# Performance work log

Measured on AMD Instinct MI355X. Metric: run time of the kernel, lower is better.

The kernel has to match this reference:

```python
import jax, jax.numpy as jnp
import numpy as np

N_SAMPLES = 131072
N_EVENTS = 128
N_ATOMS = 32
ATOM_SIZE = 512
LATENT_DIM = 16
TOTAL_LAYERS = 7  # log2(n_events)


def setup_inputs() -> dict:
    key = jax.random.key(0)
    ks = jax.random.split(key, 9)
    r = lambda k, s: jax.random.normal(k, s, dtype=jnp.float32) * 0.1
    return {
        "base_latent": r(ks[0], (1, LATENT_DIM)),
        "to_off_w": r(ks[1], (TOTAL_LAYERS, 2, LATENT_DIM)),
        "split_w": r(ks[2], (TOTAL_LAYERS, 2 * LATENT_DIM, LATENT_DIM)),
        "split_b": r(ks[3], (TOTAL_LAYERS, 2 * LATENT_DIM)),
        "atoms": r(ks[4], (N_ATOMS, ATOM_SIZE)),
        "to_atoms_w": r(ks[5], (N_ATOMS, LATENT_DIM)),
        "to_atoms_b": r(ks[6], (N_ATOMS,)),
        "to_amp_w": r(ks[7], (1, LATENT_DIM)),
        "to_amp_b": r(ks[8], (1,)),
    }


def fft_shift(a, shift):
    # FFT-based fractional delay: pad to 3*n, phase-rotate spectrum, crop.
    n = a.shape[-1]
    shift_samples = shift * n * 0.5  # shift: (B, E, 1)
    a = jnp.pad(a, [(0, 0)] * (a.ndim - 1) + [(0, n * 2)])
    spec = jnp.fft.rfft(a, axis=-1, norm="ortho")
    n_coeffs = spec.shape[-1]
    coeffs = (jnp.arange(n_coeffs) * 2j * jnp.pi) / n_coeffs  # (n_coeffs,)
    spec = spec * jnp.exp(coeffs * shift_samples)  # broadcast (B,E,n_coeffs)
    samples = jnp.fft.irfft(spec, axis=-1, norm="ortho")
    return samples[..., :n]


def _forward(base_latent, to_off_w, split_w, split_b, atoms,
             to_atoms_w, to_atoms_b, to_amp_w, to_amp_b):
    x = base_latent[:, None, :]                     # (1, 1, L)
    base_times = jnp.zeros((1, 1, 1), dtype=x.dtype)
    for i in range(TOTAL_LAYERS):
        scale = 1.0 / (2 ** i)
        b, e, _ = x.shape
        to = jax.nn.sigmoid(jnp.einsum("bel,ol->beo", x, to_off_w[i]))  # (b,e,2)
        base_times = (base_times + to * scale).reshape(b, e * 2, 1)
        split = jnp.einsum("bel,ol->beo", x, split_w[i]) + split_b[i]   # (b,e,2L)
        x = split.reshape(b, e * 2, LATENT_DIM)
    # x: (1, 128, L), base_times: (1, 128, 1)
    mix = jnp.einsum("bel,al->bea", x, to_atoms_w) + to_atoms_b          # (1,E,A)
    ev = jnp.einsum("bea,at->bet", mix, atoms)                           # (1,E,512)
    n_arr = jnp.arange(ATOM_SIZE, dtype=ev.dtype)
    window = 0.54 - 0.46 * jnp.cos(2.0 * jnp.pi * n_arr / ATOM_SIZE)     # periodic hamming
    ev = ev * window
    ev = jnp.pad(ev, ((0, 0), (0, 0), (0, N_SAMPLES - ATOM_SIZE)))       # (1,E,n_samples)
    ev = ev / (jnp.linalg.norm(ev, axis=-1, keepdims=True) + 1e-8)       # unit_norm
    amps = jnp.einsum("bel,ol->beo", x, to_amp_w) + to_amp_b             # (1,E,1)
    ev = ev * amps
    scheduled = fft_shift(ev, base_times)                                # (1,E,n_samples)
    return jnp.sum(scheduled, axis=1, keepdims=True)                     # (1,1,n_samples)


def reference(base_latent, to_off_w, split_w, split_b, atoms,
              to_atoms_w, to_atoms_b, to_amp_w, to_amp_b):
    return _forward(base_latent, to_off_w, split_w, split_b, atoms,
                    to_atoms_w, to_atoms_b, to_amp_w, to_amp_b)
```

## Files before the change

kernel.cpp:

```cpp
#include <hip/hip_runtime.h>
#include <hip/hip_bf16.h>
#include <math.h>

constexpr int NSAMP  = 131072;
constexpr int NEV    = 128;
constexpr int ASIZE  = 512;
constexpr int LDIM   = 16;
constexpr int NLAYER = 7;
constexpr int NFFT   = 393216;
constexpr int MHALF  = 196608;
constexpr double TWO_PI = 6.283185307179586;


__device__ __forceinline__ float2 cmulf(float2 a, float2 b) {
    return make_float2(a.x*b.x - a.y*b.y, a.x*b.y + a.y*b.x);
}
__device__ __forceinline__ float2 CADD(float2 a, float2 b){ return make_float2(a.x+b.x, a.y+b.y); }
__device__ __forceinline__ float2 CSUB(float2 a, float2 b){ return make_float2(a.x-b.x, a.y-b.y); }

__device__ __forceinline__ void phase_sc(float th32, float* ps, float* pc) {
    const double th = (double)th32;
    const double n  = rint(th * 0.15915494309189535);
    double r = fma(-n, 6.283185307179586, th);
    r = fma(-n, 2.4492935982947064e-16, r);
    __sincosf((float)r, ps, pc);
}

#define RT2 0.70710678118654752f
#define DFT8F(A0,A1,A2,A3,A4,A5,A6,A7, X0,X1,X2,X3,X4,X5,X6,X7) { \
  float2 b0=CADD(A0,A4), b1=CADD(A1,A5), b2=CADD(A2,A6), b3=CADD(A3,A7); \
  float2 c0=CSUB(A0,A4); \
  float2 d1=CSUB(A1,A5), d2=CSUB(A2,A6), d3=CSUB(A3,A7); \
  float2 c1=make_float2((d1.x+d1.y)*RT2, (d1.y-d1.x)*RT2); \
  float2 c2=make_float2(d2.y, -d2.x); \
  float2 c3=make_float2((d3.y-d3.x)*RT2, -(d3.x+d3.y)*RT2); \
  float2 t0=CADD(b0,b2), t1=CSUB(b0,b2), t2=CADD(b1,b3), t3=CSUB(b1,b3); \
  X0=CADD(t0,t2); X4=CSUB(t0,t2); \
  X2=make_float2(t1.x+t3.y, t1.y-t3.x); X6=make_float2(t1.x-t3.y, t1.y+t3.x); \
  t0=CADD(c0,c2); t1=CSUB(c0,c2); t2=CADD(c1,c3); t3=CSUB(c1,c3); \
  X1=CADD(t0,t2); X5=CSUB(t0,t2); \
  X3=make_float2(t1.x+t3.y, t1.y-t3.x); X7=make_float2(t1.x-t3.y, t1.y+t3.x); \
}

__global__ __launch_bounds__(256) void init_all(
    const float* __restrict__ base, const float* __restrict__ to_off_w,
    const float* __restrict__ split_w, const float* __restrict__ split_b,
    float* __restrict__ xF, float* __restrict__ sF,
    float2* __restrict__ Twf, float2* __restrict__ Ttab)
{
    const int blk = blockIdx.x;
    const int tid = threadIdx.x;
    if (blk == 0) {
        __shared__ float xA[NEV*LDIM], xB[NEV*LDIM], bA[NEV], bB[NEV];
        if (tid < LDIM) xA[tid] = base[tid];
        if (tid == 0) bA[0] = 0.0f;
        __syncthreads();
        float* xi = xA; float* xo = xB; float* bi = bA; float* bo = bB;
        for (int i = 0; i < NLAYER; ++i) {
            const int ein = 1 << i;
            const float scale = 1.0f / (float)(1 << i);
            for (int idx = tid; idx < ein*32; idx += 256) {
                const int ep = idx >> 5, o2 = idx & 31;
                const float* wr = split_w + (i*32 + o2)*LDIM;
                const float* xr = xi + ep*LDIM;
                float s = __fmul_rn(xr[0], wr[0]);
                for (int l = 1; l < LDIM; ++l)
                    s = __fadd_rn(s, __fmul_rn(xr[l], wr[l]));
                s = __fadd_rn(s, split_b[i*32 + o2]);
                xo[(ep*2 + (o2>>4))*LDIM + (o2&15)] = s;
            }
            for (int idx = tid; idx < ein*2; idx += 256) {
                const int ep = idx >> 1, o = idx & 1;
                const float* wr = to_off_w + (i*2 + o)*LDIM;
                const float* xr = xi + ep*LDIM;
                float v = __fmul_rn(xr[0], wr[0]);
                for (int l = 1; l < LDIM; ++l)
                    v = __fadd_rn(v, __fmul_rn(xr[l], wr[l]));
                const float ef = (float)exp(-(double)v);
                const float sg = __fdiv_rn(1.0f, __fadd_rn(1.0f, ef));
                bo[ep*2 + o] = __fadd_rn(bi[ep], __fmul_rn(sg, scale));
            }
            __syncthreads();
            float* t;
            t = xi; xi = xo; xo = t;
            t = bi; bi = bo; bo = t;
        }
        for (int idx = tid; idx < NEV*LDIM; idx += 256) xF[idx] = xi[idx];
        for (int e = tid; e < NEV; e += 256)
            sF[e] = __fmul_rn(__fmul_rn(bi[e], 131072.0f), 0.5f);
        return;
    }
    if (blk == 1) {
        double s, c;
        sincos(TWO_PI*(double)tid/256.0,   &s, &c); Twf[tid]       = make_float2((float)c,(float)s);
        sincos(TWO_PI*(double)tid/512.0,   &s, &c); Twf[256 + tid] = make_float2((float)c,(float)s);
        sincos(TWO_PI*(double)tid/768.0,   &s, &c); Twf[512 + tid] = make_float2((float)c,(float)s);
        sincos(TWO_PI*(double)tid/65536.0, &s, &c); Twf[768 + tid] = make_float2((float)c,(float)s);
        return;
    }
    const int b = blk - 2;
    for (int j = tid; j < 512; j += 256) {
        double s, c;
        sincos(-TWO_PI*(double)(b*j)/(double)NFFT, &s, &c);
        Ttab[b*512 + (j & 63)*8 + (j >> 6)] = make_float2((float)c, (float)s);
    }
}

__global__ __launch_bounds__(256) void events_f32(
    const float* __restrict__ atoms, const float* __restrict__ to_atoms_w,
    const float* __restrict__ to_atoms_b, const float* __restrict__ to_amp_w,
    const float* __restrict__ to_amp_b, const float* __restrict__ xF,
    float* __restrict__ zf)
{
    const int e = blockIdx.x;
    const int tid = threadIdx.x;
    __shared__ float mixS[32];
    __shared__ float evS[ASIZE];
    __shared__ double red[256];
    __shared__ float scl[2];
    const float* x = xF + e*LDIM;
    if (tid < 32) {
        const float* wr = to_atoms_w + tid*LDIM;
        float m = __fmul_rn(x[0], wr[0]);
        for (int l = 1; l < LDIM; ++l) m = __fadd_rn(m, __fmul_rn(x[l], wr[l]));
        mixS[tid] = __fadd_rn(m, to_atoms_b[tid]);
    }
    __syncthreads();
    double ss = 0.0;
    for (int u = tid; u < ASIZE; u += 256) {
        float v = __fmul_rn(mixS[0], atoms[u]);
        for (int a = 1; a < 32; ++a)
            v = __fadd_rn(v, __fmul_rn(mixS[a], atoms[a*ASIZE + u]));
        const float ang = __fdiv_rn(__fmul_rn(6.283185307179586f, (float)u), 512.0f);
        const float cw = (float)cos((double)ang);
        const float w  = __fsub_rn(0.54f, __fmul_rn(0.46f, cw));
        v = __fmul_rn(v, w);
        evS[u] = v;
        ss += (double)v * (double)v;
    }
    red[tid] = ss; __syncthreads();
    for (int s = 128; s > 0; s >>= 1) { if (tid < s) red[tid] += red[tid+s]; __syncthreads(); }
    if (tid == 0) {
        const float nf = (float)sqrt(red[0]);
        scl[0] = __fadd_rn(nf, 1e-8f);
        float a = __fmul_rn(x[0], to_amp_w[0]);
        for (int l = 1; l < LDIM; ++l) a = __fadd_rn(a, __fmul_rn(x[l], to_amp_w[l]));
        scl[1] = __fadd_rn(a, to_amp_b[0]);
    }
    __syncthreads();
    const float den = scl[0], amp = scl[1];
    for (int u = tid; u < ASIZE; u += 256)
        zf[e*ASIZE + (u & 63)*8 + (u >> 6)] =
            __fmul_rn(__fdiv_rn(evS[u], den), amp);
}

__global__ __launch_bounds__(256, 3) void forward_v3(
    const float* __restrict__ zf, const float* __restrict__ sF,
    const float2* __restrict__ Ttab, float* __restrict__ Hqf)
{
    __shared__ float2 FB[4*576];
    const int b       = blockIdx.x >> 2;
    const int quarter = blockIdx.x & 3;
    const int tid  = threadIdx.x;
    const int wave = tid >> 6, lane = tid & 63;
    float2* F = FB + wave*576;
    const int e0 = quarter*32;

    const float4* Tg4 = (const float4*)(Ttab + b*512 + lane*8);
    const float4 tA = Tg4[0], tB = Tg4[1], tC = Tg4[2], tD = Tg4[3];
    const float2 T0 = make_float2(tA.x, tA.y), T1 = make_float2(tA.z, tA.w);
    const float2 T2 = make_float2(tB.x, tB.y), T3 = make_float2(tB.z, tB.w);
    const float2 T4 = make_float2(tC.x, tC.y), T5 = make_float2(tC.z, tC.w);
    const float2 T6 = make_float2(tD.x, tD.y), T7 = make_float2(tD.z, tD.w);

    float2 w0b, w1b;
    __sincosf(-6.283185307179586f/512.0f * (float)lane,        &w0b.y, &w0b.x);
    __sincosf(-6.283185307179586f/64.0f  * (float)(lane >> 3), &w1b.y, &w1b.x);

    float c2a[4], c2b[4];
    #pragma unroll
    for (int j = 0; j < 4; ++j) {
        const int a  = lane + 64*j;
        const int k1 = b + 768*a;
        const int k2 = (768 - b) + 768*(255 - a);
        c2a[j] = __fdiv_rn(__fmul_rn((float)(2*k1), 3.14159274101257324f), 196609.0f);
        c2b[j] = __fdiv_rn(__fmul_rn((float)(2*k2), 3.14159274101257324f), 196609.0f);
    }

    float a1R[4]={0,0,0,0}, a1I[4]={0,0,0,0};
    float a2R[4]={0,0,0,0}, a2I[4]={0,0,0,0};
    const int ph = lane + (lane >> 3);

    const float4* zp4 = (const float4*)(zf + (e0 + wave*8)*ASIZE + lane*8);
    float4 za = zp4[0], zb = zp4[1];

    for (int it = 0; it < 8; ++it) {
        const float sev = sF[e0 + wave*8 + it];
        {
            const float2 i0 = make_float2(za.x*T0.x, za.x*T0.y);
            const float2 i1 = make_float2(za.y*T1.x, za.y*T1.y);
            const float2 i2 = make_float2(za.z*T2.x, za.z*T2.y);
            const float2 i3 = make_float2(za.w*T3.x, za.w*T3.y);
            const float2 i4 = make_float2(zb.x*T4.x, zb.x*T4.y);
            const float2 i5 = make_float2(zb.y*T5.x, zb.y*T5.y);
            const float2 i6 = make_float2(zb.z*T6.x, zb.z*T6.y);
            const float2 i7 = make_float2(zb.w*T7.x, zb.w*T7.y);
            za = zp4[(it+1)*128];
            zb = zp4[(it+1)*128 + 1];
            float2 x0,x1,x2,x3,x4,x5,x6,x7;
            DFT8F(i0,i1,i2,i3,i4,i5,i6,i7, x0,x1,x2,x3,x4,x5,x6,x7);
            const int ob = 9*lane;
            float2 wm = w0b;
            F[ob]   = x0;
            F[ob+1] = cmulf(x1, wm); wm = cmulf(wm, w0b);
            F[ob+2] = cmulf(x2, wm); wm = cmulf(wm, w0b);
            F[ob+3] = cmulf(x3, wm); wm = cmulf(wm, w0b);
            F[ob+4] = cmulf(x4, wm); wm = cmulf(wm, w0b);
            F[ob+5] = cmulf(x5, wm); wm = cmulf(wm, w0b);
            F[ob+6] = cmulf(x6, wm); wm = cmulf(wm, w0b);
            F[ob+7] = cmulf(x7, wm);
        }
        {
            const float2 i0 = F[ph      ], i1 = F[ph +  72], i2 = F[ph + 144],
                         i3 = F[ph + 216], i4 = F[ph + 288], i5 = F[ph + 360],
                         i6 = F[ph + 432], i7 = F[ph + 504];
            float2 x0,x1,x2,x3,x4,x5,x6,x7;
            DFT8F(i0,i1,i2,i3,i4,i5,i6,i7, x0,x1,x2,x3,x4,x5,x6,x7);
            const int q = lane & 7, p = lane >> 3;
            const int ob = q + 72*p;
            float2 wm = w1b;
            F[ob]    = x0;
            F[ob+ 9] = cmulf(x1, wm); wm = cmulf(wm, w1b);
            F[ob+18] = cmulf(x2, wm); wm = cmulf(wm, w1b);
            F[ob+27] = cmulf(x3, wm); wm = cmulf(wm, w1b);
            F[ob+36] = cmulf(x4, wm); wm = cmulf(wm, w1b);
            F[ob+45] = cmulf(x5, wm); wm = cmulf(wm, w1b);
            F[ob+54] = cmulf(x6, wm); wm = cmulf(wm, w1b);
            F[ob+63] = cmulf(x7, wm);
        }
        float2 Y[8];
        {
            const float2 i0 = F[ph      ], i1 = F[ph +  72], i2 = F[ph + 144],
                         i3 = F[ph + 216], i4 = F[ph + 288], i5 = F[ph + 360],
                         i6 = F[ph + 432], i7 = F[ph + 504];
            DFT8F(i0,i1,i2,i3,i4,i5,i6,i7, Y[0],Y[1],Y[2],Y[3],Y[4],Y[5],Y[6],Y[7]);
        }
        #pragma unroll
        for (int j = 0; j < 4; ++j) {
            float ps, pc;
            const float2 S0 = Y[j];
            phase_sc(__fmul_rn(c2a[j], sev), &ps, &pc);
            a1R[j] = fmaf(S0.x, pc, fmaf(-S0.y, ps, a1R[j]));
            a1I[j] = fmaf(S0.x, ps, fmaf( S0.y, pc, a1I[j]));
            const float2 S1 = Y[j+4];
            phase_sc(__fmul_rn(c2b[j], sev), &ps, &pc);
            a2R[j] = fmaf(S1.x, pc, fmaf( S1.y, ps, a2R[j]));
            a2I[j] = fmaf(S1.x, ps, fmaf(-S1.y, pc, a2I[j]));
        }
    }

    float* redF = (float*)FB;
    #pragma unroll
    for (int round = 0; round < 2; ++round) {
        __syncthreads();
        const int j0 = 2*round;
        float* my = redF + (wave*64 + lane)*8;
        my[0]=a1R[j0];   my[1]=a1I[j0];   my[2]=a2R[j0];   my[3]=a2I[j0];
        my[4]=a1R[j0+1]; my[5]=a1I[j0+1]; my[6]=a2R[j0+1]; my[7]=a2I[j0+1];
        __syncthreads();
        const int s = tid >> 2, c = tid & 3;
        #pragma unroll
        for (int jr = 0; jr < 2; ++jr) {
            float v = 0.f;
            #pragma unroll
            for (int w = 0; w < 4; ++w) v += redF[(w*64 + s)*8 + jr*4 + c];
            const int as = s + 64*(j0 + jr);
            if (c < 2) {
                Hqf[2*(quarter*196609 + b*256 + as) + c] = v;
            } else if (b != 384) {
                if (b != 0)
                    Hqf[2*(quarter*196609 + (768-b)*256 + (255-as)) + (c-2)] = v;
                else if (as == 0)
                    Hqf[2*(quarter*196609 + 196608) + (c-2)] = v;
            }
        }
    }
}

__device__ __forceinline__ void ifft256f_stage(
    const float2* __restrict__ src, float2* __restrict__ dst, int t, int s4,
    const float2* __restrict__ Tw256f)
{
    const int lg = 2*s4, st = 1 << lg;
    const int q = t & (st-1), p = t >> lg;
    const float2 A0 = src[t], A1 = src[t+64], A2 = src[t+128], A3 = src[t+192];
    const float Pr = A0.x + A2.x, Pi_ = A0.y + A2.y;
    const float Qr = A0.x - A2.x, Qi  = A0.y - A2.y;
    const float Rr = A1.x + A3.x, Ri  = A1.y + A3.y;
    const float Sr = A1.x - A3.x, Si  = A1.y - A3.y;
    const int tw = p*st;
    const float2 w1 = Tw256f[tw];
    const float2 w2 = Tw256f[(2*tw) & 255];
    const float2 w3 = Tw256f[(3*tw) & 255];
    const int o = q + 4*st*p;
    dst[o] = make_float2(Pr + Rr, Pi_ + Ri);
    const float u1r = Qr - Si, u1i = Qi + Sr;
    dst[o + st]   = make_float2(u1r*w1.x - u1i*w1.y, u1r*w1.y + u1i*w1.x);
    const float u2r = Pr - Rr, u2i = Pi_ - Ri;
    dst[o + 2*st] = make_float2(u2r*w2.x - u2i*w2.y, u2r*w2.y + u2i*w2.x);
    const float u3r = Qr + Si, u3i = Qi - Sr;
    dst[o + 3*st] = make_float2(u3r*w3.x - u3i*w3.y, u3r*w3.y + u3i*w3.x);
}

__global__ __launch_bounds__(64) void inv_a(
    const float* __restrict__ Hqf, const float2* __restrict__ Twf,
    float2* __restrict__ Yg)
{
    __shared__ float2 buf[512];
    const int t = threadIdx.x;
    const int job = blockIdx.x;
    const int l = job >> 8, j1 = job & 255;
    const int k0 = 3*j1 + l;
    float2* A = buf; float2* B = buf + 256;
    const float2* Hq2 = (const float2*)Hqf;
    const float2* Tw256f = Twf;
    const float2* Tw512f = Twf + 256;
    const float2* Tw64kf = Twf + 768;

    double Ss, Sc; sincos(TWO_PI*(double)k0/(double)NFFT, &Ss, &Sc);
    const float Scf = (float)Sc, Ssf = (float)Ss;

    #pragma unroll
    for (int r = 0; r < 4; ++r) {
        const int j2 = t + 64*r;
        const int idxK = k0*256 + j2;
        int idxM;
        if (k0 > 0) idxM = (768 - k0)*256 + (255 - j2);
        else        idxM = (j2 == 0) ? 196608 : (256 - j2);
        float hkR=0.f, hkI=0.f, hmR=0.f, hmI=0.f;
        #pragma unroll
        for (int q = 0; q < 4; ++q) {
            const float2 vk = Hq2[q*196609 + idxK];
            const float2 vm = Hq2[q*196609 + idxM];
            hkR += vk.x; hkI += vk.y;
            hmR += vm.x; hmI += vm.y;
        }
        if (k0 == 0 && j2 == 0) { hkI = 0.f; hmI = 0.f; }
        const float Pr = hkR + hmR, Pi_ = hkI - hmI;
        const float Qr = hkR - hmR, Qi = hkI + hmI;
        const float2 t5 = Tw512f[j2];
        const float Wc = Scf*t5.x - Ssf*t5.y;
        const float Wsn = Scf*t5.y + Ssf*t5.x;
        const float WQr = Wc*Qr - Wsn*Qi;
        const float WQi = Wc*Qi + Wsn*Qr;
        A[j2] = make_float2(0.5f*(Pr - WQi), 0.5f*(Pi_ + WQr));
    }

    ifft256f_stage(A, B, t, 0, Tw256f);
    ifft256f_stage(B, A, t, 1, Tw256f);
    ifft256f_stage(A, B, t, 2, Tw256f);
    ifft256f_stage(B, A, t, 3, Tw256f);

    #pragma unroll
    for (int r = 0; r < 4; ++r) {
        const int m1 = t + 64*r;
        const float2 v = A[m1];
        const int vv = j1*m1;
        const float2 wa = Tw256f[vv >> 8];
        const float2 wb = Tw64kf[vv & 255];
        const float twc = wa.x*wb.x - wa.y*wb.y;
        const float tws = wa.x*wb.y + wa.y*wb.x;
        Yg[m1*768 + job] = make_float2(v.x*twc - v.y*tws, v.x*tws + v.y*twc);
    }
}

__global__ __launch_bounds__(192) void inv_b(
    const float2* __restrict__ Yg, const float2* __restrict__ Twf,
    float* __restrict__ out)
{
    __shared__ float2 buf[3*512];
    const int m1 = blockIdx.x;
    const int tid = threadIdx.x;
    const int l = tid >> 6, t = tid & 63;
    const float2* Tw256f = Twf;
    const float2* Tw768f = Twf + 512;
    {
        float2* A = buf + l*512;
        float2* B = A + 256;
        #pragma unroll
        for (int r = 0; r < 4; ++r) {
            const int j1 = t + 64*r;
            A[j1] = Yg[m1*768 + l*256 + j1];
        }
        ifft256f_stage(A, B, t, 0, Tw256f);
        ifft256f_stage(B, A, t, 1, Tw256f);
        ifft256f_stage(A, B, t, 2, Tw256f);
        ifft256f_stage(B, A, t, 3, Tw256f);
    }
    __syncthreads();

    double smd, cmd; sincos(TWO_PI*(double)m1/(double)MHALF, &smd, &cmd);
    const float cm = (float)cmd, sm = (float)smd;
    const float inv = 1.0f/(float)MHALF;
    for (int m2 = tid; m2 < 256; m2 += 192) {
        const float2 F0 = buf[m2];
        const float2 F1 = buf[512 + m2];
        const float2 F2 = buf[1024 + m2];
        const float2 t7 = Tw768f[m2];
        const float w1c = cm*t7.x - sm*t7.y, w1s = cm*t7.y + sm*t7.x;
        const float w2c = w1c*w1c - w1s*w1s, w2s = 2.0f*w1c*w1s;
        const float gr = F0.x + (w1c*F1.x - w1s*F1.y) + (w2c*F2.x - w2s*F2.y);
        const float gi = F0.y + (w1c*F1.y + w1s*F1.x) + (w2c*F2.y + w2s*F2.x);
        const int m = m1 + 256*m2;
        out[2*m]     = gr*inv;
        out[2*m + 1] = gi*inv;
    }
}

extern "C" void kernel_launch(void* const* d_in, const int* in_sizes, int n_in,
                              void* d_out, int out_size, void* d_ws, size_t ws_size,
                              hipStream_t stream) {
    const float* base       = (const float*)d_in[0];
    const float* to_off_w   = (const float*)d_in[1];
    const float* split_w    = (const float*)d_in[2];
    const float* split_b    = (const float*)d_in[3];
    const float* atoms      = (const float*)d_in[4];
    const float* to_atoms_w = (const float*)d_in[5];
    const float* to_atoms_b = (const float*)d_in[6];
    const float* to_amp_w   = (const float*)d_in[7];
    const float* to_amp_b   = (const float*)d_in[8];
    float* out = (float*)d_out;

    char* ws = (char*)d_ws;
    float2* Twf  = (float2*)(ws + 0);
    float*  sF   = (float*)(ws + 8192);
    float*  xF   = (float*)(ws + 8704);
    float*  zf   = (float*)(ws + 16896);
    float2* Ttab = (float2*)(ws + 279040);
    float2* Yg   = (float2*)(ws + 279040);
    float*  Hqf  = (float*)(ws + 1856000);

    init_all<<<387, 256, 0, stream>>>(base, to_off_w, split_w, split_b,
                                      xF, sF, Twf, Ttab);
    events_f32<<<NEV, 256, 0, stream>>>(atoms, to_atoms_w, to_atoms_b,
                                        to_amp_w, to_amp_b, xF, zf);
    forward_v3<<<385*4, 256, 0, stream>>>(zf, sF, Ttab, Hqf);
    inv_a<<<768, 64, 0, stream>>>(Hqf, Twf, Yg);
    inv_b<<<256, 192, 0, stream>>>(Yg, Twf, out);
}
```

Before: 136.8 us.

## Fuse latent tree walk into events kernel and precompute per-block twiddles

Merges the init and events kernels into one launch. Each event block now recomputes its own path down the binary split tree (7 small matvecs) instead of waiting on a single block that builds all 128 latents. The double-precision sincos calls in inv_a and inv_b are replaced by lookups into small Tk/Tm tables filled by the init block. This removes one kernel launch and a serial single-block dependency, at the cost of redundant per-event tree computation and more global table reads.

```diff
diff --git a/kernel.cpp b/kernel.cpp
--- a/kernel.cpp
+++ b/kernel.cpp
@@ -42,87 +42,87 @@
   X3=make_float2(t1.x+t3.y, t1.y-t3.x); X7=make_float2(t1.x-t3.y, t1.y+t3.x); \
 }
 
-__global__ __launch_bounds__(256) void init_all(
+__global__ __launch_bounds__(256) void init_events(
     const float* __restrict__ base, const float* __restrict__ to_off_w,
     const float* __restrict__ split_w, const float* __restrict__ split_b,
-    float* __restrict__ xF, float* __restrict__ sF,
-    float2* __restrict__ Twf, float2* __restrict__ Ttab)
+    const float* __restrict__ atoms, const float* __restrict__ to_atoms_w,
+    const float* __restrict__ to_atoms_b, const float* __restrict__ to_amp_w,
+    const float* __restrict__ to_amp_b,
+    float* __restrict__ sF, float2* __restrict__ Twf,
+    float2* __restrict__ Ttab,
+    float2* __restrict__ Tk, float2* __restrict__ Tm,
+    float* __restrict__ zf)
 {
     const int blk = blockIdx.x;
     const int tid = threadIdx.x;
-    if (blk == 0) {
-        __shared__ float xA[NEV*LDIM], xB[NEV*LDIM], bA[NEV], bB[NEV];
-        if (tid < LDIM) xA[tid] = base[tid];
-        if (tid == 0) bA[0] = 0.0f;
-        __syncthreads();
-        float* xi = xA; float* xo = xB; float* bi = bA; float* bo = bB;
-        for (int i = 0; i < NLAYER; ++i) {
-            const int ein = 1 << i;
-            const float scale = 1.0f / (float)(1 << i);
-            for (int idx = tid; idx < ein*32; idx += 256) {
-                const int ep = idx >> 5, o2 = idx & 31;
-                const float* wr = split_w + (i*32 + o2)*LDIM;
-                const float* xr = xi + ep*LDIM;
-                float s = __fmul_rn(xr[0], wr[0]);
-                for (int l = 1; l < LDIM; ++l)
-                    s = __fadd_rn(s, __fmul_rn(xr[l], wr[l]));
-                s = __fadd_rn(s, split_b[i*32 + o2]);
-                xo[(ep*2 + (o2>>4))*LDIM + (o2&15)] = s;
-            }
-            for (int idx = tid; idx < ein*2; idx += 256) {
-                const int ep = idx >> 1, o = idx & 1;
-                const float* wr = to_off_w + (i*2 + o)*LDIM;
-                const float* xr = xi + ep*LDIM;
-                float v = __fmul_rn(xr[0], wr[0]);
-                for (int l = 1; l < LDIM; ++l)
-                    v = __fadd_rn(v, __fmul_rn(xr[l], wr[l]));
-                const float ef = (float)exp(-(double)v);
-                const float sg = __fdiv_rn(1.0f, __fadd_rn(1.0f, ef));
-                bo[ep*2 + o] = __fadd_rn(bi[ep], __fmul_rn(sg, scale));
-            }
-            __syncthreads();
-            float* t;
-            t = xi; xi = xo; xo = t;
-            t = bi; bi = bo; bo = t;
-        }
-        for (int idx = tid; idx < NEV*LDIM; idx += 256) xF[idx] = xi[idx];
-        for (int e = tid; e < NEV; e += 256)
-            sF[e] = __fmul_rn(__fmul_rn(bi[e], 131072.0f), 0.5f);
+    if (blk < 385) {
+        const int b = blk;
+        for (int j = tid; j < 512; j += 256) {
+            double s, c;
+            sincos(-TWO_PI*(double)(b*j)/(double)NFFT, &s, &c);
+            Ttab[b*512 + (j & 63)*8 + (j >> 6)] = make_float2((float)c, (float)s);
+        }
         return;
     }
-    if (blk == 1) {
+    if (blk == 385) {
         double s, c;
         sincos(TWO_PI*(double)tid/256.0,   &s, &c); Twf[tid]       = make_float2((float)c,(float)s);
         sincos(TWO_PI*(double)tid/512.0,   &s, &c); Twf[256 + tid] = make_float2((float)c,(float)s);
         sincos(TWO_PI*(double)tid/768.0,   &s, &c); Twf[512 + tid] = make_float2((float)c,(float)s);
         sincos(TWO_PI*(double)tid/65536.0, &s, &c); Twf[768 + tid] = make_float2((float)c,(float)s);
+        for (int k0 = tid; k0 < 768; k0 += 256) {
+            sincos(TWO_PI*(double)k0/(double)NFFT, &s, &c);
+            Tk[k0] = make_float2((float)c, (float)s);
+        }
+        {
+            sincos(TWO_PI*(double)tid/(double)MHALF, &s, &c);
+            Tm[tid] = make_float2((float)c, (float)s);
+        }
         return;
     }
-    const int b = blk - 2;
-    for (int j = tid; j < 512; j += 256) {
-        double s, c;
-        sincos(-TWO_PI*(double)(b*j)/(double)NFFT, &s, &c);
-        Ttab[b*512 + (j & 63)*8 + (j >> 6)] = make_float2((float)c, (float)s);
-    }
-}
-
-__global__ __launch_bounds__(256) void events_f32(
-    const float* __restrict__ atoms, const float* __restrict__ to_atoms_w,
-    const float* __restrict__ to_atoms_b, const float* __restrict__ to_amp_w,
-    const float* __restrict__ to_amp_b, const float* __restrict__ xF,
-    float* __restrict__ zf)
-{
-    const int e = blockIdx.x;
-    const int tid = threadIdx.x;
+
+    const int e = blk - 386;
+    __shared__ float xcur[LDIM], xnxt[LDIM];
+    __shared__ float btS;
     __shared__ float mixS[32];
     __shared__ float evS[ASIZE];
     __shared__ double red[256];
     __shared__ float scl[2];
-    const float* x = xF + e*LDIM;
+
+    if (tid < LDIM) xcur[tid] = base[tid];
+    if (tid == 0) btS = 0.0f;
+    __syncthreads();
+    for (int i = 0; i < NLAYER; ++i) {
+        const int j = (e >> (6 - i)) & 1;
+        const float scale = 1.0f / (float)(1 << i);
+        if (tid < LDIM) {
+            const float* wr = split_w + (i*32 + j*16 + tid)*LDIM;
+            float s = __fmul_rn(xcur[0], wr[0]);
+            for (int l = 1; l < LDIM; ++l)
+                s = __fadd_rn(s, __fmul_rn(xcur[l], wr[l]));
+            s = __fadd_rn(s, split_b[i*32 + j*16 + tid]);
+            xnxt[tid] = s;
+        }
+        if (tid == 64) {
+            const float* wr = to_off_w + (i*2 + j)*LDIM;
+            float v = __fmul_rn(xcur[0], wr[0]);
+            for (int l = 1; l < LDIM; ++l)
+                v = __fadd_rn(v, __fmul_rn(xcur[l], wr[l]));
+            const float ef = (float)exp(-(double)v);
+            const float sg = __fdiv_rn(1.0f, __fadd_rn(1.0f, ef));
+            btS = __fadd_rn(btS, __fmul_rn(sg, scale));
+        }
+        __syncthreads();
+        if (tid < LDIM) xcur[tid] = xnxt[tid];
+        __syncthreads();
+    }
+    if (tid == 0)
+        sF[e] = __fmul_rn(__fmul_rn(btS, 131072.0f), 0.5f);
+
     if (tid < 32) {
         const float* wr = to_atoms_w + tid*LDIM;
-        float m = __fmul_rn(x[0], wr[0]);
-        for (int l = 1; l < LDIM; ++l) m = __fadd_rn(m, __fmul_rn(x[l], wr[l]));
+        float m = __fmul_rn(xcur[0], wr[0]);
+        for (int l = 1; l < LDIM; ++l) m = __fadd_rn(m, __fmul_rn(xcur[l], wr[l]));
         mixS[tid] = __fadd_rn(m, to_atoms_b[tid]);
     }
     __syncthreads();
@@ -143,8 +143,8 @@
     if (tid == 0) {
         const float nf = (float)sqrt(red[0]);
         scl[0] = __fadd_rn(nf, 1e-8f);
-        float a = __fmul_rn(x[0], to_amp_w[0]);
-        for (int l = 1; l < LDIM; ++l) a = __fadd_rn(a, __fmul_rn(x[l], to_amp_w[l]));
+        float a = __fmul_rn(xcur[0], to_amp_w[0]);
+        for (int l = 1; l < LDIM; ++l) a = __fadd_rn(a, __fmul_rn(xcur[l], to_amp_w[l]));
         scl[1] = __fadd_rn(a, to_amp_b[0]);
     }
     __syncthreads();
@@ -314,7 +314,7 @@
 
 __global__ __launch_bounds__(64) void inv_a(
     const float* __restrict__ Hqf, const float2* __restrict__ Twf,
-    float2* __restrict__ Yg)
+    const float2* __restrict__ Tk, float2* __restrict__ Yg)
 {
     __shared__ float2 buf[512];
     const int t = threadIdx.x;
@@ -327,8 +327,8 @@
     const float2* Tw512f = Twf + 256;
     const float2* Tw64kf = Twf + 768;
 
-    double Ss, Sc; sincos(TWO_PI*(double)k0/(double)NFFT, &Ss, &Sc);
-    const float Scf = (float)Sc, Ssf = (float)Ss;
+    const float2 tkv = Tk[k0];
+    const float Scf = tkv.x, Ssf = tkv.y;
 
     #pragma unroll
     for (int r = 0; r < 4; ++r) {
@@ -376,7 +376,7 @@
 
 __global__ __launch_bounds__(192) void inv_b(
     const float2* __restrict__ Yg, const float2* __restrict__ Twf,
-    float* __restrict__ out)
+    const float2* __restrict__ Tm, float* __restrict__ out)
 {
     __shared__ float2 buf[3*512];
     const int m1 = blockIdx.x;
@@ -399,8 +399,8 @@
     }
     __syncthreads();
 
-    double smd, cmd; sincos(TWO_PI*(double)m1/(double)MHALF, &smd, &cmd);
-    const float cm = (float)cmd, sm = (float)smd;
+    const float2 tmv = Tm[m1];
+    const float cm = tmv.x, sm = tmv.y;
     const float inv = 1.0f/(float)MHALF;
     for (int m2 = tid; m2 < 256; m2 += 192) {
         const float2 F0 = buf[m2];
@@ -434,17 +434,18 @@
     char* ws = (char*)d_ws;
     float2* Twf  = (float2*)(ws + 0);
     float*  sF   = (float*)(ws + 8192);
-    float*  xF   = (float*)(ws + 8704);
+    float2* Tk   = (float2*)(ws + 8704);
+    float2* Tm   = (float2*)(ws + 14848);
     float*  zf   = (float*)(ws + 16896);
     float2* Ttab = (float2*)(ws + 279040);
     float2* Yg   = (float2*)(ws + 279040);
     float*  Hqf  = (float*)(ws + 1856000);
 
-    init_all<<<387, 256, 0, stream>>>(base, to_off_w, split_w, split_b,
-                                      xF, sF, Twf, Ttab);
-    events_f32<<<NEV, 256, 0, stream>>>(atoms, to_atoms_w, to_atoms_b,
-                                        to_amp_w, to_amp_b, xF, zf);
+    init_events<<<514, 256, 0, stream>>>(base, to_off_w, split_w, split_b,
+                                         atoms, to_atoms_w, to_atoms_b,
+                                         to_amp_w, to_amp_b,
+                                         sF, Twf, Ttab, Tk, Tm, zf);
     forward_v3<<<385*4, 256, 0, stream>>>(zf, sF, Ttab, Hqf);
-    inv_a<<<768, 64, 0, stream>>>(Hqf, Twf, Yg);
-    inv_b<<<256, 192, 0, stream>>>(Yg, Twf, out);
-}
+    inv_a<<<768, 64, 0, stream>>>(Hqf, Twf, Tk, Yg);
+    inv_b<<<256, 192, 0, stream>>>(Yg, Twf, Tm, out);
+}
```

Measured after the change: 132.5 us (median of 2 runs). -3.1%, faster.
